# Kernel optimization log

Measured on AMD Instinct MI355X. Metric: run time of the kernel, lower is better.

Reference implementation:

```python
import jax, jax.numpy as jnp
import numpy as np

LN_EPS = 1e-5

def silu(x):
    return x * jax.nn.sigmoid(x)

def setup_inputs() -> dict:
    key = jax.random.key(0)
    ks = jax.random.split(key, 24)
    B, D = 131072, 256
    def w(k, shape, fan_in):
        return jax.random.uniform(k, shape, jnp.float32, -1.0, 1.0) / np.sqrt(fan_in)
    inp = {
        'x': jax.random.normal(ks[0], (B, D), jnp.float32),
        # stem: Linear(D,128) -> LN(128) -> SiLU -> Linear(128,64) -> SiLU
        'stem_w1': w(ks[1], (D, 128), D), 'stem_b1': w(ks[2], (128,), D),
        'ln_g': jnp.ones((128,), jnp.float32), 'ln_b': jnp.zeros((128,), jnp.float32),
        'stem_w2': w(ks[3], (128, 64), 128), 'stem_b2': w(ks[4], (64,), 128),
        # 4 experts: Linear(64,128)->SiLU->Linear(128,64)->SiLU, stacked on axis 0
        'ew1': w(ks[5], (4, 64, 128), 64), 'eb1': w(ks[6], (4, 128), 64),
        'ew2': w(ks[7], (4, 128, 64), 128), 'eb2': w(ks[8], (4, 64), 128),
        # gate: Linear(64,32)->SiLU->Linear(32,4)
        'gw1': w(ks[9], (64, 32), 64), 'gb1': w(ks[10], (32,), 64),
        'gw2': w(ks[11], (32, 4), 32), 'gb2': w(ks[12], (4,), 32),
        # shared: Linear(64,64)->SiLU
        'sw': w(ks[13], (64, 64), 64), 'sb': w(ks[14], (64,), 64),
        # 3 heads (strain, tensile, yield) stacked: Linear(64,32)->SiLU->Linear(32,1)
        'hw1': w(ks[15], (3, 64, 32), 64), 'hb1': w(ks[16], (3, 32), 64),
        'hw2': w(ks[17], (3, 32, 1), 32), 'hb2': w(ks[18], (3, 1), 32),
    }
    return inp

def reference(x, stem_w1, stem_b1, ln_g, ln_b, stem_w2, stem_b2,
              ew1, eb1, ew2, eb2, gw1, gb1, gw2, gb2, sw, sb,
              hw1, hb1, hw2, hb2):
    # stem (dropout = identity, eval mode)
    h = x @ stem_w1 + stem_b1                      # [B,128]
    mu = jnp.mean(h, -1, keepdims=True)
    var = jnp.mean(jnp.square(h - mu), -1, keepdims=True)
    h = (h - mu) * jax.lax.rsqrt(var + LN_EPS) * ln_g + ln_b
    h = silu(h)
    h = silu(h @ stem_w2 + stem_b2)                # [B,64]
    # gate
    g = silu(h @ gw1 + gb1)
    gate_w = jax.nn.softmax(g @ gw2 + gb2, axis=-1)  # [B,4]
    # experts: [B,64] x [4,64,128] -> [B,4,128]
    e = silu(jnp.einsum('bd,edh->beh', h, ew1) + eb1)
    e = silu(jnp.einsum('beh,ehd->bed', e, ew2) + eb2)  # [B,4,64]
    moe_h = jnp.einsum('bed,be->bd', e, gate_w)    # [B,64]
    # shared trunk (dropout = identity)
    feat = silu(moe_h @ sw + sb)                   # [B,64]
    # 3 heads
    hh = silu(jnp.einsum('bd,kdh->bkh', feat, hw1) + hb1)  # [B,3,32]
    out = (jnp.einsum('bkh,kho->bko', hh, hw2) + hb2)[..., 0]  # [B,3]
    return out
```

## Files before the change

kernel.cpp:

```cpp
#include <hip/hip_runtime.h>

typedef _Float16 f16;
typedef f16   f16x4 __attribute__((ext_vector_type(4)));
typedef f16   f16x8 __attribute__((ext_vector_type(8)));
typedef float f32x4 __attribute__((ext_vector_type(4)));
typedef __attribute__((address_space(3))) char as3char;

#define MFMA16(a, b, c) __builtin_amdgcn_mfma_f32_16x16x32_f16((a), (b), (c), 0, 0, 0)

#define IMG_W1   0
#define IMG_W2   32768
#define IMG_GW1  40960
#define IMG_E    43008
#define IMG_SWH  108544

__device__ __forceinline__ float silu_f(float v) {
    return v * __builtin_amdgcn_rcpf(1.0f + __expf(-v));
}

__device__ void conv_blk(const float* __restrict__ src, f16* __restrict__ dst,
                         int srcN, int k0, int n0, int KB, int NB, int tid, int nth) {
    for (int i = tid; i < KB * NB; i += nth) {
        const int kk = i / NB, nn = i - kk * NB;
        dst[nn * KB + (kk ^ ((nn & 7) << 3))] = (f16)src[(long)(k0 + kk) * srcN + n0 + nn];
    }
}

__global__ void prep_weights(const float* __restrict__ w1, const float* __restrict__ w2,
                             const float* __restrict__ gw1, const float* __restrict__ ew1,
                             const float* __restrict__ ew2, const float* __restrict__ sw,
                             const float* __restrict__ hw1, f16* __restrict__ ws) {
    const int tid = blockIdx.x * 256 + threadIdx.x;
    const int nth = gridDim.x * 256;
    for (int kq = 0; kq < 4; ++kq)
        for (int nh = 0; nh < 2; ++nh)
            conv_blk(w1, ws + IMG_W1 + (kq * 2 + nh) * 4096, 128, kq * 64, nh * 64, 64, 64, tid, nth);
    for (int kh = 0; kh < 2; ++kh)
        conv_blk(w2, ws + IMG_W2 + kh * 4096, 64, kh * 64, 0, 64, 64, tid, nth);
    conv_blk(gw1, ws + IMG_GW1, 32, 0, 0, 64, 32, tid, nth);
    for (int e = 0; e < 4; ++e)
        for (int h = 0; h < 2; ++h) {
            conv_blk(ew1 + e * 8192, ws + IMG_E + e * 16384 + h * 8192,        128, 0, h * 64, 64, 64, tid, nth);
            conv_blk(ew2 + e * 8192, ws + IMG_E + e * 16384 + h * 8192 + 4096,  64, h * 64, 0, 64, 64, tid, nth);
        }
    conv_blk(sw, ws + IMG_SWH, 64, 0, 0, 64, 64, tid, nth);
    for (int h = 0; h < 3; ++h)
        conv_blk(hw1 + h * 2048, ws + IMG_SWH + 4096 + h * 2048, 32, 0, 0, 64, 32, tid, nth);
}

template<int BYTES>
__device__ __forceinline__ void stage4(const f16* __restrict__ g, as3char* l, int wv, int lane) {
    constexpr int CH = BYTES / 1024;
    #pragma unroll
    for (int ch = 0; ch < CH; ++ch)
        if ((ch & 3) == wv)
            __builtin_amdgcn_global_load_lds(
                (const __attribute__((address_space(1))) void*)((const char*)g + ch * 1024 + lane * 16),
                (__attribute__((address_space(3))) void*)(l + ch * 1024), 16, 0, 0);
}

__device__ __forceinline__ int swzW(int n) { return (n & 7) << 3; }
__device__ __forceinline__ int swzS(int r) { return (((((r >> 2) & 3) << 1) | (r & 1))) << 3; }

__device__ __forceinline__ f16x8 ldW(const f16* base, int row_base, int k0, int lane) {
    const int r = row_base + (lane & 15);
    const int k = k0 + ((lane >> 4) << 3);
    return *(const f16x8*)(base + r * 64 + (k ^ swzW(r)));
}
__device__ __forceinline__ f16x8 ldS(const f16* strip, int k0, int lane) {
    const int r = lane & 15;
    const int k = k0 + ((lane >> 4) << 3);
    return *(const f16x8*)(strip + r * 64 + (k ^ swzS(r)));
}
__device__ __forceinline__ void stS(f16* strip, int col_base, f32x4 v, int lane) {
    const int cc = col_base + (lane & 15);
    #pragma unroll
    for (int g = 0; g < 4; ++g) {
        const int r = ((lane >> 4) << 2) + g;
        strip[r * 64 + (cc ^ swzS(r))] = (f16)v[g];
    }
}

__device__ __forceinline__ void mm8(const f16x8 a[2], const f16* wb, f32x4 acc[4], int lane) {
    #pragma unroll
    for (int ks = 0; ks < 2; ++ks)
        #pragma unroll
        for (int n = 0; n < 4; ++n) {
            const f16x8 b = ldW(wb, n * 16, ks * 32, lane);
            acc[n] = MFMA16(a[ks], b, acc[n]);
        }
}

__device__ __forceinline__ void silu_to_frags(f16* strip, const f32x4 in[4], f16x8 outf[2], int lane) {
    #pragma unroll
    for (int n = 0; n < 4; ++n) {
        f32x4 v;
        #pragma unroll
        for (int g = 0; g < 4; ++g) v[g] = silu_f(in[n][g]);
        stS(strip, n * 16, v, lane);
    }
    #pragma unroll
    for (int ks = 0; ks < 2; ++ks)
        outf[ks] = ldS(strip, ks * 32, lane);
}

__device__ __forceinline__ f32x4 reduce16(f32x4 v) {
    #pragma unroll
    for (int m = 1; m <= 8; m <<= 1) {
        f32x4 o;
        #pragma unroll
        for (int i = 0; i < 4; ++i) o[i] = __shfl_xor(v[i], m, 64);
        v += o;
    }
    return v;
}

__global__ __launch_bounds__(256, 4)
void fused_net_mfma(const float* __restrict__ x,   const f16* __restrict__ wsp,
                    const float* __restrict__ b1,  const float* __restrict__ lng,
                    const float* __restrict__ lnb, const float* __restrict__ b2,
                    const float* __restrict__ eb1, const float* __restrict__ eb2,
                    const float* __restrict__ gb1, const float* __restrict__ gw2,
                    const float* __restrict__ gb2, const float* __restrict__ sb,
                    const float* __restrict__ hb1, const float* __restrict__ hw2,
                    const float* __restrict__ hb2, float* __restrict__ out)
{
    __shared__ __align__(16) f16 lds[22784];
    as3char* const LB = (as3char*)lds;
    const int lane = threadIdx.x & 63;
    const int wv   = threadIdx.x >> 6;
    const int c    = lane & 15;
    const int q    = lane >> 4;
    f16* STRIP = lds + wv * 1024;
    f16* const WA = lds + 4096;   as3char* const WA_3 = LB + 8192;
    f16* const WB = lds + 12288;  as3char* const WB_3 = LB + 24576;
    f16* const G  = lds + 20480;  as3char* const G_3  = LB + 40960;
    f16* const GWT = lds + 22528;

    const long blockRow = (long)blockIdx.x * 64;
    const float* xw = x + (blockRow + wv * 16) * 256;

    stage4<16384>(wsp + IMG_W1, WA_3, wv, lane);
    stage4<4096>(wsp + IMG_GW1, G_3, wv, lane);
    float4 xr[4];
    #pragma unroll
    for (int i = 0; i < 4; ++i) {
        const int idx4 = lane + i * 64;
        xr[i] = *(const float4*)(xw + (idx4 >> 4) * 256 + ((idx4 & 15) << 2));
    }
    __syncthreads();

    f32x4 acc[8];
    #pragma unroll
    for (int n8 = 0; n8 < 8; ++n8) {
        const float bv = b1[n8 * 16 + c];
        f32x4 t = {bv, bv, bv, bv};
        acc[n8] = t;
    }

    #pragma unroll
    for (int kq = 0; kq < 4; ++kq) {
        const f16* cur  = (kq & 1) ? WB : WA;
        as3char* nxt3   = (kq & 1) ? WA_3 : WB_3;
        if (kq < 3) stage4<16384>(wsp + IMG_W1 + (kq + 1) * 8192, nxt3, wv, lane);
        else        stage4<16384>(wsp + IMG_W2, nxt3, wv, lane);
        #pragma unroll
        for (int i = 0; i < 4; ++i) {
            const int idx4 = lane + i * 64;
            const int r  = idx4 >> 4;
            const int c4 = (idx4 & 15) << 2;
            f16x4 o; o[0] = (f16)xr[i].x; o[1] = (f16)xr[i].y; o[2] = (f16)xr[i].z; o[3] = (f16)xr[i].w;
            *(f16x4*)(STRIP + r * 64 + (c4 ^ swzS(r))) = o;
        }
        f16x8 af[2];
        #pragma unroll
        for (int ks = 0; ks < 2; ++ks)
            af[ks] = ldS(STRIP, ks * 32, lane);
        if (kq < 3) {
            #pragma unroll
            for (int i = 0; i < 4; ++i) {
                const int idx4 = lane + i * 64;
                xr[i] = *(const float4*)(xw + (idx4 >> 4) * 256 + (kq + 1) * 64 + ((idx4 & 15) << 2));
            }
        }
        mm8(af, cur,        acc,     lane);
        mm8(af, cur + 4096, acc + 4, lane);
        __syncthreads();
    }

    f32x4 mu, rs;
    {
        f32x4 s = {0,0,0,0}, qq = {0,0,0,0};
        #pragma unroll
        for (int n8 = 0; n8 < 8; ++n8) { s += acc[n8]; qq += acc[n8] * acc[n8]; }
        s = reduce16(s); qq = reduce16(qq);
        mu = s * 0.0078125f;
        #pragma unroll
        for (int g = 0; g < 4; ++g)
            rs[g] = rsqrtf(qq[g] * 0.0078125f - mu[g] * mu[g] + 1e-5f);
    }

    stage4<16384>(wsp + IMG_E, WB_3, wv, lane);
    f32x4 a2[4];
    #pragma unroll
    for (int n = 0; n < 4; ++n) {
        const float bv = b2[n * 16 + c];
        f32x4 t = {bv, bv, bv, bv};
        a2[n] = t;
    }
    #pragma unroll
    for (int kh = 0; kh < 2; ++kh) {
        #pragma unroll
        for (int n = 0; n < 4; ++n) {
            const int j = kh * 64 + n * 16 + c;
            const float gg = lng[j], bb = lnb[j];
            f32x4 v;
            #pragma unroll
            for (int g = 0; g < 4; ++g)
                v[g] = silu_f((acc[kh * 4 + n][g] - mu[g]) * rs[g] * gg + bb);
            stS(STRIP, n * 16, v, lane);
        }
        f16x8 af[2];
        #pragma unroll
        for (int ks = 0; ks < 2; ++ks)
            af[ks] = ldS(STRIP, ks * 32, lane);
        mm8(af, WA + kh * 4096, a2, lane);
    }
    f16x8 hbA[2];
    silu_to_frags(STRIP, a2, hbA, lane);

    {
        f32x4 ag[2];
        #pragma unroll
        for (int n = 0; n < 2; ++n) {
            const float bv = gb1[n * 16 + c];
            f32x4 t = {bv, bv, bv, bv};
            ag[n] = t;
        }
        #pragma unroll
        for (int ks = 0; ks < 2; ++ks)
            #pragma unroll
            for (int n = 0; n < 2; ++n) {
                const f16x8 b = ldW(G, n * 16, ks * 32, lane);
                ag[n] = MFMA16(hbA[ks], b, ag[n]);
            }
        const f32x4 gb2v = *(const f32x4*)gb2;
        f32x4 pg[4] = {{0,0,0,0},{0,0,0,0},{0,0,0,0},{0,0,0,0}};
        #pragma unroll
        for (int n = 0; n < 2; ++n) {
            const f32x4 w4 = *(const f32x4*)(gw2 + (n * 16 + c) * 4);
            #pragma unroll
            for (int g = 0; g < 4; ++g)
                pg[g] += silu_f(ag[n][g]) * w4;
        }
        #pragma unroll
        for (int g = 0; g < 4; ++g) {
            f32x4 l = reduce16(pg[g]) + gb2v;
            const float mx = fmaxf(fmaxf(l[0], l[1]), fmaxf(l[2], l[3]));
            f32x4 ee;
            #pragma unroll
            for (int o = 0; o < 4; ++o) ee[o] = __expf(l[o] - mx);
            const f32x4 gv = ee * __builtin_amdgcn_rcpf(ee[0] + ee[1] + ee[2] + ee[3]);
            if (c < 4) {
                const float val = (c == 0) ? gv[0] : (c == 1) ? gv[1] : (c == 2) ? gv[2] : gv[3];
                GWT[wv * 64 + c * 16 + q * 4 + g] = (f16)val;
            }
        }
    }
    __syncthreads();

    f32x4 moe[4] = {{0,0,0,0},{0,0,0,0},{0,0,0,0},{0,0,0,0}};
    #pragma unroll 1
    for (int e = 0; e < 4; ++e) {
        f32x4 a2e[4];
        #pragma unroll
        for (int n = 0; n < 4; ++n) {
            const float bv = eb2[e * 64 + n * 16 + c];
            f32x4 t = {bv, bv, bv, bv};
            a2e[n] = t;
        }
        stage4<16384>(wsp + IMG_E + e * 16384 + 8192, WA_3, wv, lane);
        {
            f32x4 aa[4];
            #pragma unroll
            for (int n = 0; n < 4; ++n) {
                const float bv = eb1[e * 128 + n * 16 + c];
                f32x4 t = {bv, bv, bv, bv};
                aa[n] = t;
            }
            mm8(hbA, WB, aa, lane);
            f16x8 ea[2];
            silu_to_frags(STRIP, aa, ea, lane);
            mm8(ea, WB + 4096, a2e, lane);
        }
        __syncthreads();
        if (e < 3) stage4<16384>(wsp + IMG_E + (e + 1) * 16384, WB_3, wv, lane);
        else       stage4<12288>(wsp + IMG_SWH, WB_3, wv, lane);
        {
            f32x4 aa[4];
            #pragma unroll
            for (int n = 0; n < 4; ++n) {
                const float bv = eb1[e * 128 + 64 + n * 16 + c];
                f32x4 t = {bv, bv, bv, bv};
                aa[n] = t;
            }
            mm8(hbA, WA, aa, lane);
            f16x8 ea[2];
            silu_to_frags(STRIP, aa, ea, lane);
            mm8(ea, WA + 4096, a2e, lane);
        }
        #pragma unroll
        for (int g = 0; g < 4; ++g) {
            const float ge = (float)GWT[wv * 64 + e * 16 + q * 4 + g];
            #pragma unroll
            for (int n = 0; n < 4; ++n)
                moe[n][g] += silu_f(a2e[n][g]) * ge;
        }
        __syncthreads();
    }

    stage4<8192>(wsp + IMG_SWH + 6144, WA_3, wv, lane);
    f16x8 featA[2];
    {
        #pragma unroll
        for (int n = 0; n < 4; ++n)
            stS(STRIP, n * 16, moe[n], lane);
        f16x8 ma[2];
        #pragma unroll
        for (int ks = 0; ks < 2; ++ks)
            ma[ks] = ldS(STRIP, ks * 32, lane);
        f32x4 fs[4];
        #pragma unroll
        for (int n = 0; n < 4; ++n) {
            const float bv = sb[n * 16 + c];
            f32x4 t = {bv, bv, bv, bv};
            fs[n] = t;
        }
        mm8(ma, WB, fs, lane);
        silu_to_frags(STRIP, fs, featA, lane);
    }
    __syncthreads();

    {
        f32x4 ah[6];
        #pragma unroll
        for (int n = 0; n < 6; ++n) {
            const float bv = hb1[(n >> 1) * 32 + (n & 1) * 16 + c];
            f32x4 t = {bv, bv, bv, bv};
            ah[n] = t;
        }
        #pragma unroll
        for (int ks = 0; ks < 2; ++ks)
            #pragma unroll
            for (int n = 0; n < 6; ++n) {
                const int h = n >> 1;
                const f16* hw = (h == 0) ? (WB + 4096) : (h == 1) ? WA : (WA + 2048);
                const f16x8 b = ldW(hw, (n & 1) * 16, ks * 32, lane);
                ah[n] = MFMA16(featA[ks], b, ah[n]);
            }
        const float hb2_0 = hb2[0], hb2_1 = hb2[1], hb2_2 = hb2[2];
        f32x4 ph[3] = {{0,0,0,0},{0,0,0,0},{0,0,0,0}};
        #pragma unroll
        for (int n = 0; n < 6; ++n) {
            const int h = n >> 1;
            const float w2v = hw2[h * 32 + (n & 1) * 16 + c];
            #pragma unroll
            for (int g = 0; g < 4; ++g)
                ph[h][g] += silu_f(ah[n][g]) * w2v;
        }
        #pragma unroll
        for (int h = 0; h < 3; ++h) ph[h] = reduce16(ph[h]);
        #pragma unroll
        for (int g = 0; g < 4; ++g) {
            const long row = blockRow + wv * 16 + q * 4 + g;
            if (c < 3) {
                const float r0 = ph[0][g] + hb2_0;
                const float r1 = ph[1][g] + hb2_1;
                const float r2 = ph[2][g] + hb2_2;
                out[row * 3 + c] = (c == 0) ? r0 : ((c == 1) ? r1 : r2);
            }
        }
    }
}

extern "C" void kernel_launch(void* const* d_in, const int* in_sizes, int n_in,
                              void* d_out, int out_size, void* d_ws, size_t ws_size,
                              hipStream_t stream) {
    const float* x    = (const float*)d_in[0];
    const float* w1   = (const float*)d_in[1];
    const float* b1   = (const float*)d_in[2];
    const float* lng  = (const float*)d_in[3];
    const float* lnb  = (const float*)d_in[4];
    const float* w2   = (const float*)d_in[5];
    const float* b2   = (const float*)d_in[6];
    const float* ew1  = (const float*)d_in[7];
    const float* eb1  = (const float*)d_in[8];
    const float* ew2  = (const float*)d_in[9];
    const float* eb2  = (const float*)d_in[10];
    const float* gw1  = (const float*)d_in[11];
    const float* gb1  = (const float*)d_in[12];
    const float* gw2  = (const float*)d_in[13];
    const float* gb2  = (const float*)d_in[14];
    const float* sw   = (const float*)d_in[15];
    const float* sb   = (const float*)d_in[16];
    const float* hw1  = (const float*)d_in[17];
    const float* hb1  = (const float*)d_in[18];
    const float* hw2  = (const float*)d_in[19];
    const float* hb2  = (const float*)d_in[20];
    float* out = (float*)d_out;
    f16* ws = (f16*)d_ws;

    hipLaunchKernelGGL(prep_weights, dim3(64), dim3(256), 0, stream,
                       w1, w2, gw1, ew1, ew2, sw, hw1, ws);

    const int B = in_sizes[0] / 256;
    const int grid = B / 64;
    hipLaunchKernelGGL(fused_net_mfma, dim3(grid), dim3(256), 0, stream,
                       x, ws, b1, lng, lnb, b2, eb1, eb2, gb1, gw2, gb2,
                       sb, hb1, hw2, hb2, out);
}
```

Baseline: 120.7 us.

## Halve LDS weight buffers to 8KB chunks to raise occupancy

Shrinks the shared-memory footprint from about 45KB to about 29KB by staging weights in 4096-element halves instead of 8192-element tiles. The double-buffered schedule is rewritten throughout the stem, expert and head phases to ping-pong between the two smaller buffers. The goal is to fit more blocks per CU so global-memory latency is better hidden. In exchange it adds roughly twice as many __syncthreads barriers and staging steps per block, and the stem loop is no longer unrolled.

```diff
diff --git a/kernel.cpp b/kernel.cpp
--- a/kernel.cpp
+++ b/kernel.cpp
@@ -125,7 +125,7 @@
                     const float* __restrict__ hb1, const float* __restrict__ hw2,
                     const float* __restrict__ hb2, float* __restrict__ out)
 {
-    __shared__ __align__(16) f16 lds[22784];
+    __shared__ __align__(16) f16 lds[14592];
     as3char* const LB = (as3char*)lds;
     const int lane = threadIdx.x & 63;
     const int wv   = threadIdx.x >> 6;
@@ -133,14 +133,14 @@
     const int q    = lane >> 4;
     f16* STRIP = lds + wv * 1024;
     f16* const WA = lds + 4096;   as3char* const WA_3 = LB + 8192;
-    f16* const WB = lds + 12288;  as3char* const WB_3 = LB + 24576;
-    f16* const G  = lds + 20480;  as3char* const G_3  = LB + 40960;
-    f16* const GWT = lds + 22528;
+    f16* const WB = lds + 8192;   as3char* const WB_3 = LB + 16384;
+    f16* const G  = lds + 12288;  as3char* const G_3  = LB + 24576;
+    f16* const GWT = lds + 14336;
 
     const long blockRow = (long)blockIdx.x * 64;
     const float* xw = x + (blockRow + wv * 16) * 256;
 
-    stage4<16384>(wsp + IMG_W1, WA_3, wv, lane);
+    stage4<8192>(wsp + IMG_W1, WA_3, wv, lane);
     stage4<4096>(wsp + IMG_GW1, G_3, wv, lane);
     float4 xr[4];
     #pragma unroll
@@ -158,12 +158,14 @@
         acc[n8] = t;
     }
 
-    #pragma unroll
+    #pragma unroll 1
     for (int kq = 0; kq < 4; ++kq) {
-        const f16* cur  = (kq & 1) ? WB : WA;
-        as3char* nxt3   = (kq & 1) ? WA_3 : WB_3;
-        if (kq < 3) stage4<16384>(wsp + IMG_W1 + (kq + 1) * 8192, nxt3, wv, lane);
-        else        stage4<16384>(wsp + IMG_W2, nxt3, wv, lane);
+        const f16* curA = (kq & 1) ? WB : WA;
+        as3char* othA   = (kq & 1) ? WA_3 : WB_3;
+        const f16* curB = (kq & 1) ? WA : WB;
+        as3char* othB   = (kq & 1) ? WB_3 : WA_3;
+
+        stage4<8192>(wsp + IMG_W1 + (kq * 2 + 1) * 4096, othA, wv, lane);
         #pragma unroll
         for (int i = 0; i < 4; ++i) {
             const int idx4 = lane + i * 64;
@@ -176,6 +178,11 @@
         #pragma unroll
         for (int ks = 0; ks < 2; ++ks)
             af[ks] = ldS(STRIP, ks * 32, lane);
+        mm8(af, curA, acc, lane);
+        __syncthreads();
+
+        if (kq < 3) stage4<8192>(wsp + IMG_W1 + (kq + 1) * 2 * 4096, othB, wv, lane);
+        else        stage4<8192>(wsp + IMG_W2, othB, wv, lane);
         if (kq < 3) {
             #pragma unroll
             for (int i = 0; i < 4; ++i) {
@@ -183,8 +190,7 @@
                 xr[i] = *(const float4*)(xw + (idx4 >> 4) * 256 + (kq + 1) * 64 + ((idx4 & 15) << 2));
             }
         }
-        mm8(af, cur,        acc,     lane);
-        mm8(af, cur + 4096, acc + 4, lane);
+        mm8(af, curB, acc + 4, lane);
         __syncthreads();
     }
 
@@ -200,7 +206,6 @@
             rs[g] = rsqrtf(qq[g] * 0.0078125f - mu[g] * mu[g] + 1e-5f);
     }
 
-    stage4<16384>(wsp + IMG_E, WB_3, wv, lane);
     f32x4 a2[4];
     #pragma unroll
     for (int n = 0; n < 4; ++n) {
@@ -208,28 +213,46 @@
         f32x4 t = {bv, bv, bv, bv};
         a2[n] = t;
     }
-    #pragma unroll
-    for (int kh = 0; kh < 2; ++kh) {
+    stage4<8192>(wsp + IMG_W2 + 4096, WB_3, wv, lane);
+    {
         #pragma unroll
         for (int n = 0; n < 4; ++n) {
-            const int j = kh * 64 + n * 16 + c;
+            const int j = n * 16 + c;
             const float gg = lng[j], bb = lnb[j];
             f32x4 v;
             #pragma unroll
             for (int g = 0; g < 4; ++g)
-                v[g] = silu_f((acc[kh * 4 + n][g] - mu[g]) * rs[g] * gg + bb);
+                v[g] = silu_f((acc[n][g] - mu[g]) * rs[g] * gg + bb);
             stS(STRIP, n * 16, v, lane);
         }
         f16x8 af[2];
         #pragma unroll
         for (int ks = 0; ks < 2; ++ks)
             af[ks] = ldS(STRIP, ks * 32, lane);
-        mm8(af, WA + kh * 4096, a2, lane);
-    }
+        mm8(af, WA, a2, lane);
+    }
+    __syncthreads();
+
+    stage4<8192>(wsp + IMG_E, WA_3, wv, lane);
     f16x8 hbA[2];
-    silu_to_frags(STRIP, a2, hbA, lane);
-
     {
+        #pragma unroll
+        for (int n = 0; n < 4; ++n) {
+            const int j = 64 + n * 16 + c;
+            const float gg = lng[j], bb = lnb[j];
+            f32x4 v;
+            #pragma unroll
+            for (int g = 0; g < 4; ++g)
+                v[g] = silu_f((acc[4 + n][g] - mu[g]) * rs[g] * gg + bb);
+            stS(STRIP, n * 16, v, lane);
+        }
+        f16x8 af[2];
+        #pragma unroll
+        for (int ks = 0; ks < 2; ++ks)
+            af[ks] = ldS(STRIP, ks * 32, lane);
+        mm8(af, WB, a2, lane);
+        silu_to_frags(STRIP, a2, hbA, lane);
+
         f32x4 ag[2];
         #pragma unroll
         for (int n = 0; n < 2; ++n) {
@@ -272,6 +295,7 @@
     f32x4 moe[4] = {{0,0,0,0},{0,0,0,0},{0,0,0,0},{0,0,0,0}};
     #pragma unroll 1
     for (int e = 0; e < 4; ++e) {
+        const f16* ebase = wsp + IMG_E + e * 16384;
         f32x4 a2e[4];
         #pragma unroll
         for (int n = 0; n < 4; ++n) {
@@ -279,7 +303,8 @@
             f32x4 t = {bv, bv, bv, bv};
             a2e[n] = t;
         }
-        stage4<16384>(wsp + IMG_E + e * 16384 + 8192, WA_3, wv, lane);
+        f16x8 ea[2];
+        stage4<8192>(ebase + 4096, WB_3, wv, lane);
         {
             f32x4 aa[4];
             #pragma unroll
@@ -288,14 +313,14 @@
                 f32x4 t = {bv, bv, bv, bv};
                 aa[n] = t;
             }
-            mm8(hbA, WB, aa, lane);
-            f16x8 ea[2];
+            mm8(hbA, WA, aa, lane);
             silu_to_frags(STRIP, aa, ea, lane);
-            mm8(ea, WB + 4096, a2e, lane);
-        }
-        __syncthreads();
-        if (e < 3) stage4<16384>(wsp + IMG_E + (e + 1) * 16384, WB_3, wv, lane);
-        else       stage4<12288>(wsp + IMG_SWH, WB_3, wv, lane);
+        }
+        __syncthreads();
+        stage4<8192>(ebase + 8192, WA_3, wv, lane);
+        mm8(ea, WB, a2e, lane);
+        __syncthreads();
+        stage4<8192>(ebase + 8192 + 4096, WB_3, wv, lane);
         {
             f32x4 aa[4];
             #pragma unroll
@@ -305,10 +330,12 @@
                 aa[n] = t;
             }
             mm8(hbA, WA, aa, lane);
-            f16x8 ea[2];
             silu_to_frags(STRIP, aa, ea, lane);
-            mm8(ea, WA + 4096, a2e, lane);
-        }
+        }
+        __syncthreads();
+        if (e < 3) stage4<8192>(wsp + IMG_E + (e + 1) * 16384, WA_3, wv, lane);
+        else       stage4<8192>(wsp + IMG_SWH, WA_3, wv, lane);
+        mm8(ea, WB, a2e, lane);
         #pragma unroll
         for (int g = 0; g < 4; ++g) {
             const float ge = (float)GWT[wv * 64 + e * 16 + q * 4 + g];
@@ -319,7 +346,8 @@
         __syncthreads();
     }
 
-    stage4<8192>(wsp + IMG_SWH + 6144, WA_3, wv, lane);
+    stage4<8192>(wsp + IMG_SWH + 4096, WB_3, wv, lane);
+    stage4<4096>(wsp + IMG_SWH + 8192, G_3, wv, lane);
     f16x8 featA[2];
     {
         #pragma unroll
@@ -336,7 +364,7 @@
             f32x4 t = {bv, bv, bv, bv};
             fs[n] = t;
         }
-        mm8(ma, WB, fs, lane);
+        mm8(ma, WA, fs, lane);
         silu_to_frags(STRIP, fs, featA, lane);
     }
     __syncthreads();
@@ -354,7 +382,7 @@
             #pragma unroll
             for (int n = 0; n < 6; ++n) {
                 const int h = n >> 1;
-                const f16* hw = (h == 0) ? (WB + 4096) : (h == 1) ? WA : (WA + 2048);
+                const f16* hw = (h == 0) ? WB : (h == 1) ? (WB + 2048) : G;
                 const f16x8 b = ldW(hw, (n & 1) * 16, ks * 32, lane);
                 ah[n] = MFMA16(featA[ks], b, ah[n]);
             }
```

Result: faster. 102.3 us (-15.2%).
